# Optimization experiments

Measured on AMD Instinct MI355X. Metric: run time of the kernel, lower is better.

The kernel has to match this reference:

```python
import jax, jax.numpy as jnp
import numpy as np

EPS = 1e-5

def layer_norm(x, w, b):
    mu = jnp.mean(x, axis=-1, keepdims=True)
    var = jnp.mean(jnp.square(x - mu), axis=-1, keepdims=True)
    return (x - mu) * jax.lax.rsqrt(var + EPS) * w + b

def setup_inputs() -> dict:
    key = jax.random.key(0)
    ks = jax.random.split(key, 16)
    B, N, c_z, c_h = 1, 512, 128, 128
    s_z = 1.0 / np.sqrt(c_z)
    s_h = 1.0 / np.sqrt(c_h)
    return {
        "z": jax.random.normal(ks[0], (B, N, N, c_z), jnp.float32),
        "mask": jnp.ones((B, N, N), jnp.float32),
        "norm_in_w": jnp.ones((c_z,), jnp.float32),
        "norm_in_b": jnp.zeros((c_z,), jnp.float32),
        "a_p_w": jax.random.normal(ks[1], (c_h, c_z), jnp.float32) * s_z,
        "a_p_b": jnp.zeros((c_h,), jnp.float32),
        "a_g_w": jax.random.normal(ks[2], (c_h, c_z), jnp.float32) * s_z,
        "a_g_b": jnp.ones((c_h,), jnp.float32),
        "b_p_w": jax.random.normal(ks[3], (c_h, c_z), jnp.float32) * s_z,
        "b_p_b": jnp.zeros((c_h,), jnp.float32),
        "b_g_w": jax.random.normal(ks[4], (c_h, c_z), jnp.float32) * s_z,
        "b_g_b": jnp.ones((c_h,), jnp.float32),
        "g_w": jax.random.normal(ks[5], (c_z, c_z), jnp.float32) * s_z,
        "g_b": jnp.ones((c_z,), jnp.float32),
        "z_w": jax.random.normal(ks[6], (c_z, c_h), jnp.float32) * s_h,
        "z_b": jnp.zeros((c_z,), jnp.float32),
        "norm_out_w": jnp.ones((c_h,), jnp.float32),
        "norm_out_b": jnp.zeros((c_h,), jnp.float32),
    }

OUTGOING = True

def reference(z, mask, norm_in_w, norm_in_b, a_p_w, a_p_b, a_g_w, a_g_b,
              b_p_w, b_p_b, b_g_w, b_g_b, g_w, g_b, z_w, z_b,
              norm_out_w, norm_out_b):
    # z: [B, N, N, c_z]; mask: [B, N, N]
    m = mask[..., None]  # [B, N, N, 1]
    zn = layer_norm(z, norm_in_w, norm_in_b)
    # gated projections (nn.Linear layout: W is [out, in])
    a = m * jax.nn.sigmoid(zn @ a_g_w.T + a_g_b) * (zn @ a_p_w.T + a_p_b)
    b = m * jax.nn.sigmoid(zn @ b_g_w.T + b_g_b) * (zn @ b_p_w.T + b_p_b)
    if OUTGOING:
        # x[i,j,c] = sum_k a[i,k,c] * b[j,k,c]
        x = jnp.einsum('bikc,bjkc->bijc', a, b)
    else:
        x = jnp.einsum('bkic,bkjc->bijc', a, b)
    x = layer_norm(x, norm_out_w, norm_out_b)
    x = x @ z_w.T + z_b
    g = jax.nn.sigmoid(zn @ g_w.T + g_b)
    return x * g
```

## Files before the change

### kernel.cpp

```cpp
#include <hip/hip_runtime.h>
#include <stddef.h>

#define NN 512
#define CC 128
#define NPOS (NN*NN)
#define CPITCH (NPOS + 512)

typedef unsigned short u16;
typedef unsigned int   u32;
typedef u16  u16x4  __attribute__((ext_vector_type(4)));
typedef u16  u16x8  __attribute__((ext_vector_type(8)));
typedef __bf16 bf16x8 __attribute__((ext_vector_type(8)));
typedef float f32x4  __attribute__((ext_vector_type(4)));

__device__ __forceinline__ float b2f(u16 u) {
    union { u32 i; float f; } w; w.i = ((u32)u) << 16; return w.f;
}
__device__ __forceinline__ u16 f2b(float f) {
    return __builtin_bit_cast(u16, (__bf16)f);
}
__device__ __forceinline__ float sigm(float x) { return 1.0f / (1.0f + __expf(-x)); }

__device__ __forceinline__ void gld16(const u16* g, u16* l) {
    __builtin_amdgcn_global_load_lds(
        (const __attribute__((address_space(1))) u32*)g,
        (__attribute__((address_space(3))) u32*)l, 16, 0, 0);
}

struct W6 { const float* p[6]; };

__global__ __launch_bounds__(256) void k0_pack(W6 w, u16* __restrict__ dst)
{
    const int i = blockIdx.x * 256 + threadIdx.x;
    const int mt = i >> 14, r = i & 16383;
    const int cb = r >> 11, ks = (r >> 9) & 3, lane = (r >> 3) & 63, j = r & 7;
    const int row = cb * 16 + (lane & 15);
    const int col = ks * 32 + (lane >> 4) * 8 + j;
    dst[i] = f2b(w.p[mt][row * 128 + col]);
}

__global__ __launch_bounds__(128) void k1_ln_proj(
    const float* __restrict__ z,  const float* __restrict__ mask,
    const float* __restrict__ wi, const float* __restrict__ bi,
    const u16* __restrict__ wpk,
    const float* __restrict__ agb, const float* __restrict__ apb,
    const float* __restrict__ bgb, const float* __restrict__ bpb,
    u16* __restrict__ a_cm, u16* __restrict__ b_cm,
    u16* __restrict__ zn_pm)
{
    __shared__ u16 zn[64][136];
    const int tid = threadIdx.x;
    const size_t p0 = (size_t)blockIdx.x * 64;

    {
        const float* zt = z + p0 * CC;
        const int g  = tid >> 5;
        const int c4 = (tid & 31) * 4;
        const f32x4 wi4 = *(const f32x4*)(wi + c4);
        const f32x4 bi4 = *(const f32x4*)(bi + c4);
        f32x4 v[16];
        #pragma unroll
        for (int h = 0; h < 16; ++h)
            v[h] = *(const f32x4*)(zt + h * 512 + tid * 4);
        #pragma unroll
        for (int h = 0; h < 16; ++h) {
            float s  = (v[h][0] + v[h][1]) + (v[h][2] + v[h][3]);
            float s2 = (v[h][0]*v[h][0] + v[h][1]*v[h][1])
                     + (v[h][2]*v[h][2] + v[h][3]*v[h][3]);
            #pragma unroll
            for (int ms = 1; ms <= 16; ms <<= 1) {
                s  += __shfl_xor(s,  ms);
                s2 += __shfl_xor(s2, ms);
            }
            const float mu   = s * (1.0f / CC);
            const float rstd = rsqrtf(s2 * (1.0f / CC) - mu * mu + 1e-5f);
            u16x4 o4;
            #pragma unroll
            for (int e = 0; e < 4; ++e) {
                const float nw = rstd * wi4[e];
                o4[e] = f2b(v[h][e] * nw + __builtin_fmaf(-mu, nw, bi4[e]));
            }
            *(u16x4*)&zn[h * 4 + g][c4] = o4;
            if (zn_pm)
                *(u16x4*)(zn_pm + (p0 + h * 4 + g) * CC + c4) = o4;
        }
    }
    __syncthreads();

    const int wave = tid >> 6, lane = tid & 63;
    const int m = lane & 15, q = lane >> 4;

    bf16x8 af[2][4];
    #pragma unroll
    for (int t = 0; t < 2; ++t)
        #pragma unroll
        for (int ks = 0; ks < 4; ++ks)
            af[t][ks] = *(const bf16x8*)&zn[wave * 32 + t * 16 + m][ks * 32 + q * 8];

    f32x4 mkv[2];
    #pragma unroll
    for (int t = 0; t < 2; ++t)
        mkv[t] = *(const f32x4*)(mask + p0 + wave * 32 + t * 16 + q * 4);

    const float* Bv[4] = { agb, apb, bgb, bpb };

    for (int cb = 0; cb < 8; ++cb) {
        const int o = cb * 16 + m;
        f32x4 res[4][2];
        #pragma unroll
        for (int mt = 0; mt < 4; ++mt) {
            const float bvv = Bv[mt][o];
            #pragma unroll
            for (int t = 0; t < 2; ++t) res[mt][t] = f32x4{ bvv, bvv, bvv, bvv };
            const u16* wp = wpk + ((size_t)((mt * 8 + cb) * 4)) * 512 + (size_t)lane * 8;
            bf16x8 wf[4];
            #pragma unroll
            for (int ks = 0; ks < 4; ++ks) wf[ks] = *(const bf16x8*)(wp + ks * 512);
            #pragma unroll
            for (int ks = 0; ks < 4; ++ks)
                #pragma unroll
                for (int t = 0; t < 2; ++t)
                    res[mt][t] = __builtin_amdgcn_mfma_f32_16x16x32_bf16(
                                   af[t][ks], wf[ks], res[mt][t], 0, 0, 0);
        }
        #pragma unroll
        for (int t = 0; t < 2; ++t) {
            u16x4 av, bv;
            #pragma unroll
            for (int r = 0; r < 4; ++r) {
                const float mk = mkv[t][r];
                av[r] = f2b(mk * sigm(res[0][t][r]) * res[1][t][r]);
                bv[r] = f2b(mk * sigm(res[2][t][r]) * res[3][t][r]);
            }
            const size_t off = (size_t)o * CPITCH + p0 + wave * 32 + t * 16 + q * 4;
            *(u16x4*)(a_cm + off) = av;
            *(u16x4*)(b_cm + off) = bv;
        }
    }
}

__global__ __launch_bounds__(256) void k2_gemm(
    const u16* __restrict__ A, const u16* __restrict__ B, u16* __restrict__ X)
{
    __shared__ u16 As[2][128][32];
    __shared__ u16 Bs[2][128][32];
    const int tid = threadIdx.x;
    const int bx  = blockIdx.x;
    const int xcd  = bx & 7;
    const int slot = bx >> 3;
    const int c    = (slot >> 4) * 8 + xcd;
    const int tile = slot & 15;
    const int i0   = (tile >> 2) * 128;
    const int j0   = (tile & 3) * 128;
    const size_t cbase = (size_t)c * CPITCH;
    const u16* Ac = A + cbase;
    const u16* Bc = B + cbase;

    const int wave = tid >> 6, lane = tid & 63;
    const int wm = wave >> 1, wn = wave & 1;
    const int m = lane & 15, q = lane >> 4;

    f32x4 acc[4][4];
    const f32x4 zero = { 0.f, 0.f, 0.f, 0.f };
    #pragma unroll
    for (int mt = 0; mt < 4; ++mt)
        #pragma unroll
        for (int nt = 0; nt < 4; ++nt) acc[mt][nt] = zero;

    #pragma unroll
    for (int ps = 0; ps < 2; ++ps) {
        const int id = ps * 256 + tid;
        const int rw = id >> 2;
        const int g  = (id & 3) ^ ((rw >> 1) & 3);
        gld16(Ac + (size_t)(i0 + rw) * NN + g * 8, &As[0][0][0] + id * 8);
        gld16(Bc + (size_t)(j0 + rw) * NN + g * 8, &Bs[0][0][0] + id * 8);
    }
    __syncthreads();

    int cur = 0;
    for (int kt = 0; kt < 16; ++kt) {
        if (kt < 15) {
            const int nb = cur ^ 1;
            #pragma unroll
            for (int ps = 0; ps < 2; ++ps) {
                const int id = ps * 256 + tid;
                const int rw = id >> 2;
                const int g  = (id & 3) ^ ((rw >> 1) & 3);
                const size_t goff = (size_t)((kt + 1) * 32 + g * 8);
                gld16(Ac + (size_t)(i0 + rw) * NN + goff, &As[nb][0][0] + id * 8);
                gld16(Bc + (size_t)(j0 + rw) * NN + goff, &Bs[nb][0][0] + id * 8);
            }
        }
        bf16x8 af[4], bf[4];
        #pragma unroll
        for (int mt = 0; mt < 4; ++mt) {
            const int row = wm * 64 + mt * 16 + m;
            const int slt = q ^ ((row >> 1) & 3);
            af[mt] = *(const bf16x8*)&As[cur][row][slt * 8];
        }
        #pragma unroll
        for (int nt = 0; nt < 4; ++nt) {
            const int row = wn * 64 + nt * 16 + m;
            const int slt = q ^ ((row >> 1) & 3);
            bf[nt] = *(const bf16x8*)&Bs[cur][row][slt * 8];
        }
        #pragma unroll
        for (int mt = 0; mt < 4; ++mt)
            #pragma unroll
            for (int nt = 0; nt < 4; ++nt)
                acc[mt][nt] = __builtin_amdgcn_mfma_f32_16x16x32_bf16(
                                af[mt], bf[nt], acc[mt][nt], 0, 0, 0);
        __syncthreads();
        cur ^= 1;
    }

    #pragma unroll
    for (int mt = 0; mt < 4; ++mt) {
        #pragma unroll
        for (int r = 0; r < 4; ++r) {
            const int i = i0 + wm * 64 + mt * 16 + q * 4 + r;
            #pragma unroll
            for (int nt = 0; nt < 4; ++nt) {
                const int j = j0 + wn * 64 + nt * 16 + m;
                X[cbase + (size_t)i * NN + j] = f2b(acc[mt][nt][r]);
            }
        }
    }
}

__global__ __launch_bounds__(256) void k3_out_zn(
    float* __restrict__ out, const u16* __restrict__ x_cm,
    const u16* __restrict__ zn_pm,
    const float* __restrict__ wo, const float* __restrict__ bo,
    const u16* __restrict__ wpk,
    const float* __restrict__ gbv, const float* __restrict__ zbv)
{
    __shared__ u16 A[128][136];
    __shared__ u16 Bt[128][136];
    const int tid = threadIdx.x;
    const size_t p0 = (size_t)blockIdx.x * 128;
    const int wave = tid >> 6, lane = tid & 63;
    const int m = lane & 15, q = lane >> 4;
    const int pl = tid >> 1, ht = tid & 1;

    {
        const int c = tid >> 1, seg = tid & 1;
        #pragma unroll
        for (int e = 0; e < 8; ++e) {
            u16x8 vv = *(const u16x8*)(x_cm + (size_t)c * CPITCH + p0 + seg * 64 + e * 8);
            *(u16x8*)&Bt[c][seg * 64 + e * 8] = vv;
        }
    }
    bf16x8 afz[2][4];
    #pragma unroll
    for (int t = 0; t < 2; ++t)
        #pragma unroll
        for (int ks = 0; ks < 4; ++ks)
            afz[t][ks] = *(const bf16x8*)(zn_pm
                           + (p0 + wave * 32 + t * 16 + m) * CC + ks * 32 + q * 8);
    __syncthreads();

    {
        float v[64];
        #pragma unroll
        for (int e = 0; e < 64; ++e) v[e] = b2f(Bt[ht * 64 + e][pl]);
        float s = 0.f, s2 = 0.f;
        #pragma unroll
        for (int e = 0; e < 64; ++e) { s += v[e]; s2 += v[e] * v[e]; }
        s  += __shfl_xor(s, 1);
        s2 += __shfl_xor(s2, 1);
        const float mu   = s * (1.0f / CC);
        const float rstd = rsqrtf(s2 * (1.0f / CC) - mu * mu + 1e-5f);
        #pragma unroll
        for (int h = 0; h < 8; ++h) {
            u16x8 o8;
            #pragma unroll
            for (int e = 0; e < 8; ++e) {
                const int c = ht * 64 + h * 8 + e;
                o8[e] = f2b((v[h * 8 + e] - mu) * rstd * wo[c] + bo[c]);
            }
            *(u16x8*)&A[pl][ht * 64 + h * 8] = o8;
        }
    }
    __syncthreads();

    bf16x8 afx[2][4];
    #pragma unroll
    for (int t = 0; t < 2; ++t)
        #pragma unroll
        for (int ks = 0; ks < 4; ++ks)
            afx[t][ks] = *(const bf16x8*)&A[wave * 32 + t * 16 + m][ks * 32 + q * 8];

    for (int cb = 0; cb < 8; ++cb) {
        const int o = cb * 16 + m;
        const float gb0 = gbv[o], zb0 = zbv[o];
        f32x4 accg[2], accx[2];
        #pragma unroll
        for (int t = 0; t < 2; ++t) {
            accg[t] = f32x4{ gb0, gb0, gb0, gb0 };
            accx[t] = f32x4{ zb0, zb0, zb0, zb0 };
        }
        const u16* wpg = wpk + ((size_t)((4 * 8 + cb) * 4)) * 512 + (size_t)lane * 8;
        const u16* wpz = wpk + ((size_t)((5 * 8 + cb) * 4)) * 512 + (size_t)lane * 8;
        bf16x8 wg[4], wz[4];
        #pragma unroll
        for (int ks = 0; ks < 4; ++ks) {
            wg[ks] = *(const bf16x8*)(wpg + ks * 512);
            wz[ks] = *(const bf16x8*)(wpz + ks * 512);
        }
        #pragma unroll
        for (int ks = 0; ks < 4; ++ks)
            #pragma unroll
            for (int t = 0; t < 2; ++t) {
                accg[t] = __builtin_amdgcn_mfma_f32_16x16x32_bf16(
                            afz[t][ks], wg[ks], accg[t], 0, 0, 0);
                accx[t] = __builtin_amdgcn_mfma_f32_16x16x32_bf16(
                            afx[t][ks], wz[ks], accx[t], 0, 0, 0);
            }
        #pragma unroll
        for (int t = 0; t < 2; ++t)
            #pragma unroll
            for (int r = 0; r < 4; ++r) {
                const size_t p = p0 + wave * 32 + t * 16 + q * 4 + r;
                out[p * CC + o] = accx[t][r] * sigm(accg[t][r]);
            }
    }
}

__global__ __launch_bounds__(256) void k3_out(
    float* __restrict__ out, const u16* __restrict__ x_cm,
    const float* __restrict__ z,
    const float* __restrict__ wi, const float* __restrict__ bi,
    const float* __restrict__ wo, const float* __restrict__ bo,
    const u16* __restrict__ wpk,
    const float* __restrict__ gbv, const float* __restrict__ zbv)
{
    __shared__ u16 A[128][136];
    __shared__ u16 Bt[128][136];
    const int tid = threadIdx.x;
    const size_t p0 = (size_t)blockIdx.x * 128;
    const int wave = tid >> 6, lane = tid & 63;
    const int m = lane & 15, q = lane >> 4;
    const int pl = tid >> 1, ht = tid & 1;

    {
        const float* zr = z + (p0 + pl) * CC + ht * 64;
        float v[64];
        #pragma unroll
        for (int h = 0; h < 16; ++h) {
            f32x4 t = *(const f32x4*)(zr + h * 4);
            #pragma unroll
            for (int e = 0; e < 4; ++e) v[h * 4 + e] = t[e];
        }
        float s = 0.f, s2 = 0.f;
        #pragma unroll
        for (int e = 0; e < 64; ++e) { s += v[e]; s2 += v[e] * v[e]; }
        s  += __shfl_xor(s, 1);
        s2 += __shfl_xor(s2, 1);
        const float mu   = s * (1.0f / CC);
        const float rstd = rsqrtf(s2 * (1.0f / CC) - mu * mu + 1e-5f);
        #pragma unroll
        for (int h = 0; h < 8; ++h) {
            u16x8 o8;
            #pragma unroll
            for (int e = 0; e < 8; ++e) {
                const int c = ht * 64 + h * 8 + e;
                o8[e] = f2b((v[h * 8 + e] - mu) * rstd * wi[c] + bi[c]);
            }
            *(u16x8*)&A[pl][ht * 64 + h * 8] = o8;
        }
    }
    {
        const int c = tid >> 1, seg = tid & 1;
        #pragma unroll
        for (int e = 0; e < 8; ++e) {
            u16x8 vv = *(const u16x8*)(x_cm + (size_t)c * CPITCH + p0 + seg * 64 + e * 8);
            *(u16x8*)&Bt[c][seg * 64 + e * 8] = vv;
        }
    }
    __syncthreads();

    bf16x8 afz[2][4];
    #pragma unroll
    for (int t = 0; t < 2; ++t)
        #pragma unroll
        for (int ks = 0; ks < 4; ++ks)
            afz[t][ks] = *(const bf16x8*)&A[wave * 32 + t * 16 + m][ks * 32 + q * 8];
    __syncthreads();

    {
        float v[64];
        #pragma unroll
        for (int e = 0; e < 64; ++e) v[e] = b2f(Bt[ht * 64 + e][pl]);
        float s = 0.f, s2 = 0.f;
        #pragma unroll
        for (int e = 0; e < 64; ++e) { s += v[e]; s2 += v[e] * v[e]; }
        s  += __shfl_xor(s, 1);
        s2 += __shfl_xor(s2, 1);
        const float mu   = s * (1.0f / CC);
        const float rstd = rsqrtf(s2 * (1.0f / CC) - mu * mu + 1e-5f);
        #pragma unroll
        for (int h = 0; h < 8; ++h) {
            u16x8 o8;
            #pragma unroll
            for (int e = 0; e < 8; ++e) {
                const int c = ht * 64 + h * 8 + e;
                o8[e] = f2b((v[h * 8 + e] - mu) * rstd * wo[c] + bo[c]);
            }
            *(u16x8*)&A[pl][ht * 64 + h * 8] = o8;
        }
    }
    __syncthreads();

    bf16x8 afx[2][4];
    #pragma unroll
    for (int t = 0; t < 2; ++t)
        #pragma unroll
        for (int ks = 0; ks < 4; ++ks)
            afx[t][ks] = *(const bf16x8*)&A[wave * 32 + t * 16 + m][ks * 32 + q * 8];

    for (int cb = 0; cb < 8; ++cb) {
        const int o = cb * 16 + m;
        const float gb0 = gbv[o], zb0 = zbv[o];
        f32x4 accg[2], accx[2];
        #pragma unroll
        for (int t = 0; t < 2; ++t) {
            accg[t] = f32x4{ gb0, gb0, gb0, gb0 };
            accx[t] = f32x4{ zb0, zb0, zb0, zb0 };
        }
        const u16* wpg = wpk + ((size_t)((4 * 8 + cb) * 4)) * 512 + (size_t)lane * 8;
        const u16* wpz = wpk + ((size_t)((5 * 8 + cb) * 4)) * 512 + (size_t)lane * 8;
        bf16x8 wg[4], wz[4];
        #pragma unroll
        for (int ks = 0; ks < 4; ++ks) {
            wg[ks] = *(const bf16x8*)(wpg + ks * 512);
            wz[ks] = *(const bf16x8*)(wpz + ks * 512);
        }
        #pragma unroll
        for (int ks = 0; ks < 4; ++ks)
            #pragma unroll
            for (int t = 0; t < 2; ++t) {
                accg[t] = __builtin_amdgcn_mfma_f32_16x16x32_bf16(
                            afz[t][ks], wg[ks], accg[t], 0, 0, 0);
                accx[t] = __builtin_amdgcn_mfma_f32_16x16x32_bf16(
                            afx[t][ks], wz[ks], accx[t], 0, 0, 0);
            }
        #pragma unroll
        for (int t = 0; t < 2; ++t)
            #pragma unroll
            for (int r = 0; r < 4; ++r) {
                const size_t p = p0 + wave * 32 + t * 16 + q * 4 + r;
                out[p * CC + o] = accx[t][r] * sigm(accg[t][r]);
            }
    }
}

extern "C" void kernel_launch(void* const* d_in, const int* in_sizes, int n_in,
                              void* d_out, int out_size, void* d_ws, size_t ws_size,
                              hipStream_t stream)
{
    const float* z    = (const float*)d_in[0];
    const float* mask = (const float*)d_in[1];
    const float* wi   = (const float*)d_in[2];
    const float* bi   = (const float*)d_in[3];
    const float* apw  = (const float*)d_in[4];
    const float* apb  = (const float*)d_in[5];
    const float* agw  = (const float*)d_in[6];
    const float* agb  = (const float*)d_in[7];
    const float* bpw  = (const float*)d_in[8];
    const float* bpb  = (const float*)d_in[9];
    const float* bgw  = (const float*)d_in[10];
    const float* bgb  = (const float*)d_in[11];
    const float* gw   = (const float*)d_in[12];
    const float* gb   = (const float*)d_in[13];
    const float* zw   = (const float*)d_in[14];
    const float* zb   = (const float*)d_in[15];
    const float* wo   = (const float*)d_in[16];
    const float* bo   = (const float*)d_in[17];

    u16* a_cm = (u16*)d_ws;
    u16* b_cm = a_cm + (size_t)CC * CPITCH;
    u16* x_cm = b_cm + (size_t)CC * CPITCH;
    u16* w_pk = x_cm + (size_t)CC * CPITCH;
    u16* zn_pm = w_pk + (size_t)6 * 16384;
    float* out = (float*)d_out;

    const size_t need_zn =
        ((size_t)CC * CPITCH * 3 + 6 * 16384 + (size_t)NPOS * CC) * sizeof(u16);
    const bool use_zn = (ws_size == 0) || (ws_size >= need_zn);
    if (!use_zn) zn_pm = nullptr;

    W6 w6; w6.p[0] = agw; w6.p[1] = apw; w6.p[2] = bgw; w6.p[3] = bpw;
    w6.p[4] = gw; w6.p[5] = zw;

    k0_pack<<<6 * 16384 / 256, 256, 0, stream>>>(w6, w_pk);
    k1_ln_proj<<<NPOS / 64, 128, 0, stream>>>(z, mask, wi, bi, w_pk,
                                              agb, apb, bgb, bpb, a_cm, b_cm, zn_pm);
    k2_gemm<<<128 * 16, 256, 0, stream>>>(a_cm, b_cm, x_cm);
    if (use_zn)
        k3_out_zn<<<NPOS / 128, 256, 0, stream>>>(out, x_cm, zn_pm, wo, bo,
                                                  w_pk, gb, zb);
    else
        k3_out<<<NPOS / 128, 256, 0, stream>>>(out, x_cm, z, wi, bi, wo, bo,
                                               w_pk, gb, zb);
}
```

Baseline: 473.3 us.

## Restructure LN+projection kernel: 512-thread blocks with per-wave channel ownership

The fused layernorm/gated-projection kernel now processes 128 positions per block with 8 waves, each wave owning one 16-channel output block. Each wave keeps its weight fragments resident in registers and loops over the 128 rows, instead of every wave streaming all 8 channel blocks of weights. The mask is staged through LDS and the weight loads are issued before the barrier to overlap with layernorm. This removes repeated weight reloads per wave and gives each block more parallelism, at the cost of higher register pressure (16 bf16x8 weight fragments per thread) and larger LDS use, which may limit occupancy.

```diff
diff --git a/kernel.cpp b/kernel.cpp
--- a/kernel.cpp
+++ b/kernel.cpp
@@ -39,7 +39,7 @@
     dst[i] = f2b(w.p[mt][row * 128 + col]);
 }
 
-__global__ __launch_bounds__(128) void k1_ln_proj(
+__global__ __launch_bounds__(512) void k1_ln_proj(
     const float* __restrict__ z,  const float* __restrict__ mask,
     const float* __restrict__ wi, const float* __restrict__ bi,
     const u16* __restrict__ wpk,
@@ -48,22 +48,24 @@
     u16* __restrict__ a_cm, u16* __restrict__ b_cm,
     u16* __restrict__ zn_pm)
 {
-    __shared__ u16 zn[64][136];
+    __shared__ u16   zn[128][136];
+    __shared__ float mk_lds[128];
     const int tid = threadIdx.x;
-    const size_t p0 = (size_t)blockIdx.x * 64;
-
-    {
-        const float* zt = z + p0 * CC;
+    const size_t p0 = (size_t)blockIdx.x * 128;
+
+    if (tid < 128) mk_lds[tid] = mask[p0 + tid];
+
+    {
         const int g  = tid >> 5;
         const int c4 = (tid & 31) * 4;
         const f32x4 wi4 = *(const f32x4*)(wi + c4);
         const f32x4 bi4 = *(const f32x4*)(bi + c4);
-        f32x4 v[16];
-        #pragma unroll
-        for (int h = 0; h < 16; ++h)
-            v[h] = *(const f32x4*)(zt + h * 512 + tid * 4);
-        #pragma unroll
-        for (int h = 0; h < 16; ++h) {
+        f32x4 v[8];
+        #pragma unroll
+        for (int h = 0; h < 8; ++h)
+            v[h] = *(const f32x4*)(z + (p0 + h * 16 + g) * CC + c4);
+        #pragma unroll
+        for (int h = 0; h < 8; ++h) {
             float s  = (v[h][0] + v[h][1]) + (v[h][2] + v[h][3]);
             float s2 = (v[h][0]*v[h][0] + v[h][1]*v[h][1])
                      + (v[h][2]*v[h][2] + v[h][3]*v[h][3]);
@@ -80,62 +82,65 @@
                 const float nw = rstd * wi4[e];
                 o4[e] = f2b(v[h][e] * nw + __builtin_fmaf(-mu, nw, bi4[e]));
             }
-            *(u16x4*)&zn[h * 4 + g][c4] = o4;
+            const int row = h * 16 + g;
+            *(u16x4*)&zn[row][c4] = o4;
             if (zn_pm)
-                *(u16x4*)(zn_pm + (p0 + h * 4 + g) * CC + c4) = o4;
-        }
-    }
-    __syncthreads();
+                *(u16x4*)(zn_pm + (p0 + row) * CC + c4) = o4;
+        }
+    }
 
     const int wave = tid >> 6, lane = tid & 63;
     const int m = lane & 15, q = lane >> 4;
-
-    bf16x8 af[2][4];
-    #pragma unroll
-    for (int t = 0; t < 2; ++t)
-        #pragma unroll
-        for (int ks = 0; ks < 4; ++ks)
-            af[t][ks] = *(const bf16x8*)&zn[wave * 32 + t * 16 + m][ks * 32 + q * 8];
-
-    f32x4 mkv[2];
-    #pragma unroll
-    for (int t = 0; t < 2; ++t)
-        mkv[t] = *(const f32x4*)(mask + p0 + wave * 32 + t * 16 + q * 4);
-
-    const float* Bv[4] = { agb, apb, bgb, bpb };
-
-    for (int cb = 0; cb < 8; ++cb) {
-        const int o = cb * 16 + m;
-        f32x4 res[4][2];
+    const int cb = wave;
+    const int o  = cb * 16 + m;
+
+    bf16x8 wreg[4][4];
+    float  bias4[4];
+    {
+        const float* Bv[4] = { agb, apb, bgb, bpb };
         #pragma unroll
         for (int mt = 0; mt < 4; ++mt) {
-            const float bvv = Bv[mt][o];
-            #pragma unroll
-            for (int t = 0; t < 2; ++t) res[mt][t] = f32x4{ bvv, bvv, bvv, bvv };
-            const u16* wp = wpk + ((size_t)((mt * 8 + cb) * 4)) * 512 + (size_t)lane * 8;
-            bf16x8 wf[4];
-            #pragma unroll
-            for (int ks = 0; ks < 4; ++ks) wf[ks] = *(const bf16x8*)(wp + ks * 512);
+            bias4[mt] = Bv[mt][o];
+            const u16* wp = wpk + ((size_t)((mt * 8 + cb) * 4)) * 512
+                                + (size_t)lane * 8;
             #pragma unroll
             for (int ks = 0; ks < 4; ++ks)
-                #pragma unroll
-                for (int t = 0; t < 2; ++t)
-                    res[mt][t] = __builtin_amdgcn_mfma_f32_16x16x32_bf16(
-                                   af[t][ks], wf[ks], res[mt][t], 0, 0, 0);
-        }
-        #pragma unroll
-        for (int t = 0; t < 2; ++t) {
-            u16x4 av, bv;
-            #pragma unroll
-            for (int r = 0; r < 4; ++r) {
-                const float mk = mkv[t][r];
-                av[r] = f2b(mk * sigm(res[0][t][r]) * res[1][t][r]);
-                bv[r] = f2b(mk * sigm(res[2][t][r]) * res[3][t][r]);
-            }
-            const size_t off = (size_t)o * CPITCH + p0 + wave * 32 + t * 16 + q * 4;
-            *(u16x4*)(a_cm + off) = av;
-            *(u16x4*)(b_cm + off) = bv;
-        }
+                wreg[mt][ks] = *(const bf16x8*)(wp + ks * 512);
+        }
+    }
+    __syncthreads();
+
+    #pragma unroll 2
+    for (int t = 0; t < 8; ++t) {
+        bf16x8 af[4];
+        #pragma unroll
+        for (int ks = 0; ks < 4; ++ks)
+            af[ks] = *(const bf16x8*)&zn[t * 16 + m][ks * 32 + q * 8];
+        const f32x4 mk4 = *(const f32x4*)&mk_lds[t * 16 + q * 4];
+
+        f32x4 res[4];
+        #pragma unroll
+        for (int mt = 0; mt < 4; ++mt) {
+            const float bv = bias4[mt];
+            res[mt] = f32x4{ bv, bv, bv, bv };
+        }
+        #pragma unroll
+        for (int ks = 0; ks < 4; ++ks)
+            #pragma unroll
+            for (int mt = 0; mt < 4; ++mt)
+                res[mt] = __builtin_amdgcn_mfma_f32_16x16x32_bf16(
+                            af[ks], wreg[mt][ks], res[mt], 0, 0, 0);
+
+        u16x4 av, bv;
+        #pragma unroll
+        for (int r = 0; r < 4; ++r) {
+            const float mk = mk4[r];
+            av[r] = f2b(mk * sigm(res[0][r]) * res[1][r]);
+            bv[r] = f2b(mk * sigm(res[2][r]) * res[3][r]);
+        }
+        const size_t off = (size_t)o * CPITCH + p0 + t * 16 + q * 4;
+        *(u16x4*)(a_cm + off) = av;
+        *(u16x4*)(b_cm + off) = bv;
     }
 }
 
@@ -494,8 +499,8 @@
     w6.p[4] = gw; w6.p[5] = zw;
 
     k0_pack<<<6 * 16384 / 256, 256, 0, stream>>>(w6, w_pk);
-    k1_ln_proj<<<NPOS / 64, 128, 0, stream>>>(z, mask, wi, bi, w_pk,
-                                              agb, apb, bgb, bpb, a_cm, b_cm, zn_pm);
+    k1_ln_proj<<<NPOS / 128, 512, 0, stream>>>(z, mask, wi, bi, w_pk,
+                                               agb, apb, bgb, bpb, a_cm, b_cm, zn_pm);
     k2_gemm<<<128 * 16, 256, 0, stream>>>(a_cm, b_cm, x_cm);
     if (use_zn)
         k3_out_zn<<<NPOS / 128, 256, 0, stream>>>(out, x_cm, zn_pm, wo, bo,
```

Result: no change. 481.1 us (+1.7%).
